# Kernel tuning notes

Hardware: AMD Instinct MI355X
Metric: run time of the kernel (lower is better)

Reference implementation:

```python
import jax, jax.numpy as jnp
import numpy as np

B, S, E, H, FF = 2, 2048, 768, 12, 3072
D = E // H
EPS = 1e-5


def setup_inputs() -> dict:
    key = jax.random.key(0)
    ks = jax.random.split(key, 12)
    sc = lambda n: 1.0 / np.sqrt(n)
    return {
        "x": jax.random.normal(ks[0], (B, S, E), jnp.float32),
        "wq": jax.random.normal(ks[1], (E, E), jnp.float32) * sc(E),
        "wk": jax.random.normal(ks[2], (E, E), jnp.float32) * sc(E),
        "wv": jax.random.normal(ks[3], (E, E), jnp.float32) * sc(E),
        "wo": jax.random.normal(ks[4], (E, E), jnp.float32) * sc(E),
        "bo": jax.random.normal(ks[5], (E,), jnp.float32) * 0.02,
        "w1": jax.random.normal(ks[6], (FF, E), jnp.float32) * sc(E),
        "b1": jax.random.normal(ks[7], (FF,), jnp.float32) * 0.02,
        "w2": jax.random.normal(ks[8], (E, FF), jnp.float32) * sc(FF),
        "b2": jax.random.normal(ks[9], (E,), jnp.float32) * 0.02,
        "gamma": jnp.ones((E,), jnp.float32),
        "beta": jnp.zeros((E,), jnp.float32),
    }


def _layernorm(x, g, b):
    mu = jnp.mean(x, axis=-1, keepdims=True)
    var = jnp.mean(jnp.square(x - mu), axis=-1, keepdims=True)
    return (x - mu) * jax.lax.rsqrt(var + EPS) * g + b


def reference(x, wq, wk, wv, wo, bo, w1, b1, w2, b2, gamma, beta):
    res = x
    xn = _layernorm(x, gamma, beta)
    # Q/K/V projections (torch Linear: y = x @ W.T), split into heads
    q = (xn @ wq.T).reshape(B, S, H, D)
    k = (xn @ wk.T).reshape(B, S, H, D)
    v = (xn @ wv.T).reshape(B, S, H, D)
    scale = jnp.sqrt(jnp.float32(D))
    scores = jnp.einsum("bqhd,bkhd->bhqk", q, k) / scale  # [B,H,S,S]
    causal = jnp.tril(jnp.ones((S, S), bool))
    scores = jnp.where(causal, scores, -jnp.inf)
    w = jax.nn.softmax(scores, axis=-1)
    attn = jnp.einsum("bhqk,bkhd->bqhd", w, v).reshape(B, S, E)
    attn = attn @ wo.T + bo
    res = res + attn
    y = _layernorm(res, gamma, beta)  # NOTE: same LayerNorm params reused (as in source)
    h = jax.nn.gelu(y @ w1.T + b1, approximate=False)  # nn.GELU default is exact erf
    ffn = h @ w2.T + b2
    return res + ffn
```

## Files before the change

### kernel.cpp

```cpp
#include <hip/hip_runtime.h>
#include <hip/hip_bf16.h>
#include <math.h>

typedef __bf16 bf16_8 __attribute__((ext_vector_type(8)));
typedef __bf16 bf16_4 __attribute__((ext_vector_type(4)));
typedef float f32x4 __attribute__((ext_vector_type(4)));

#define AS1 __attribute__((address_space(1)))
#define AS3 __attribute__((address_space(3)))

__global__ __launch_bounds__(256) void ln_kernel(
    const float* __restrict__ x, const float* __restrict__ g,
    const float* __restrict__ b, __hip_bfloat16* __restrict__ out, int cols) {
  const int row = blockIdx.x;
  const int t = threadIdx.x;
  float loc[3];
  float s = 0.f, s2 = 0.f;
#pragma unroll
  for (int i = 0; i < 3; ++i) {
    float v = x[(size_t)row * cols + t + i * 256];
    loc[i] = v;
    s += v;
    s2 += v * v;
  }
#pragma unroll
  for (int off = 32; off; off >>= 1) {
    s += __shfl_down(s, off);
    s2 += __shfl_down(s2, off);
  }
  __shared__ float red[2][4];
  const int lane = t & 63, w = t >> 6;
  if (lane == 0) {
    red[0][w] = s;
    red[1][w] = s2;
  }
  __syncthreads();
  s = red[0][0] + red[0][1] + red[0][2] + red[0][3];
  s2 = red[1][0] + red[1][1] + red[1][2] + red[1][3];
  const float mu = s / cols;
  const float var = s2 / cols - mu * mu;
  const float rs = rsqrtf(var + 1e-5f);
  __hip_bfloat16* orow = out + (size_t)row * cols;
#pragma unroll
  for (int i = 0; i < 3; ++i) {
    int c = t + i * 256;
    orow[c] = __hip_bfloat16((loc[i] - mu) * rs * g[c] + b[c]);
  }
}

__global__ __launch_bounds__(256) void reduce_ln(
    const float* __restrict__ x, const float* __restrict__ part, int nz,
    const float* __restrict__ bias, const float* __restrict__ g,
    const float* __restrict__ b, float* __restrict__ res,
    __hip_bfloat16* __restrict__ yout) {
  const int row = blockIdx.x;
  const int t = threadIdx.x;
  const size_t zstride = (size_t)4096 * 768;
  float loc[3];
  float s = 0.f, s2 = 0.f;
#pragma unroll
  for (int i = 0; i < 3; ++i) {
    const int c = t + i * 256;
    const size_t off = (size_t)row * 768 + c;
    float v = x[off] + bias[c];
    for (int z = 0; z < nz; ++z) v += part[(size_t)z * zstride + off];
    res[off] = v;
    loc[i] = v;
    s += v;
    s2 += v * v;
  }
#pragma unroll
  for (int off = 32; off; off >>= 1) {
    s += __shfl_down(s, off);
    s2 += __shfl_down(s2, off);
  }
  __shared__ float red[2][4];
  const int lane = t & 63, w = t >> 6;
  if (lane == 0) {
    red[0][w] = s;
    red[1][w] = s2;
  }
  __syncthreads();
  s = red[0][0] + red[0][1] + red[0][2] + red[0][3];
  s2 = red[1][0] + red[1][1] + red[1][2] + red[1][3];
  const float mu = s / 768.f;
  const float var = s2 / 768.f - mu * mu;
  const float rs = rsqrtf(var + 1e-5f);
#pragma unroll
  for (int i = 0; i < 3; ++i) {
    const int c = t + i * 256;
    yout[(size_t)row * 768 + c] = __hip_bfloat16((loc[i] - mu) * rs * g[c] + b[c]);
  }
}

__global__ __launch_bounds__(256) void reduce_out(
    const float* __restrict__ part, int nz, const float* __restrict__ bias,
    float* __restrict__ res) {
  const int row = blockIdx.x;
  const int t = threadIdx.x;
  const size_t zstride = (size_t)4096 * 768;
#pragma unroll
  for (int i = 0; i < 3; ++i) {
    const int c = t + i * 256;
    const size_t off = (size_t)row * 768 + c;
    float v = res[off] + bias[c];
    for (int z = 0; z < nz; ++z) v += part[(size_t)z * zstride + off];
    res[off] = v;
  }
}

__global__ __launch_bounds__(256) void cvt_multi(
    const float* __restrict__ sa, const float* __restrict__ sb,
    const float* __restrict__ sc, const float* __restrict__ sd,
    __hip_bfloat16* __restrict__ da, __hip_bfloat16* __restrict__ db,
    __hip_bfloat16* __restrict__ dc, __hip_bfloat16* __restrict__ dd) {
  const float* src;
  __hip_bfloat16* dst;
  if (blockIdx.y == 0) { src = sa; dst = da; }
  else if (blockIdx.y == 1) { src = sb; dst = db; }
  else if (blockIdx.y == 2) { src = sc; dst = dc; }
  else { src = sd; dst = dd; }
  const size_t i = ((size_t)blockIdx.x * 256 + threadIdx.x) * 4;
  float4 f = *(const float4*)(src + i);
  bf16_4 o;
  o[0] = (__bf16)f.x; o[1] = (__bf16)f.y; o[2] = (__bf16)f.z; o[3] = (__bf16)f.w;
  *(bf16_4*)((__bf16*)dst + i) = o;
}

__global__ __launch_bounds__(256) void transpose_v(
    const __hip_bfloat16* __restrict__ v, __hip_bfloat16* __restrict__ vt) {
  const int S = 2048, E = 768, H = 12;
  const int s0 = blockIdx.x * 64;
  const int bh = blockIdx.y;
  const int b = bh / H, h = bh - b * H;
  __shared__ __align__(16) __bf16 T[64 * 72];
  const int tid = threadIdx.x;
#pragma unroll
  for (int u = 0; u < 2; ++u) {
    int i = tid + u * 256;
    int sr = i >> 3, c = i & 7;
    *(bf16_8*)(&T[sr * 72 + c * 8]) =
        *(const bf16_8*)(v + ((size_t)b * S + s0 + sr) * E + h * 64 + c * 8);
  }
  __syncthreads();
#pragma unroll
  for (int u = 0; u < 2; ++u) {
    int i = tid + u * 256;
    int dr = i >> 3, kc = i & 7;
    bf16_8 o;
#pragma unroll
    for (int e = 0; e < 8; ++e) o[e] = T[(kc * 8 + e) * 72 + dr];
    *(bf16_8*)(vt + ((size_t)bh * 64 + dr) * S + s0 + kc * 8) = o;
  }
}

template <int MODE, bool BF32>
__global__ __launch_bounds__(256) void gemm_bt(
    const __hip_bfloat16* __restrict__ A, const void* __restrict__ Bx,
    const float* __restrict__ bias, void* __restrict__ out,
    int M, int N, int K, int lda, int ldb, int ldout) {
  constexpr int BM = 128, BN = 128, BK = 64;
  constexpr int LDBP = BF32 ? 72 : BK;
  __shared__ __align__(16) __bf16 As[2][BM * BK];
  __shared__ __align__(16) __bf16 Bs[2][BN * LDBP];
  const int tid = threadIdx.x;
  const int m0 = blockIdx.y * BM;
  const int n0 = blockIdx.x * BN;
  const int wave = tid >> 6;
  const int lane = tid & 63;
  const int quad = lane >> 4;
  const int l16 = lane & 15;
  const int wm = (wave & 1) * 64;
  const int wn = (wave >> 1) * 64;

  int kbase = 0, kcnt = K;
  if constexpr (MODE == 2 || MODE == 3) {
    kcnt = K / gridDim.z;
    kbase = blockIdx.z * kcnt;
  }
  const int nt = kcnt / BK;

  const int srow = lane >> 3;
  const int scol = ((lane & 7) ^ (srow & 7)) * 8;
  const __hip_bfloat16* Ap = A + (size_t)(m0 + wave * 8 + srow) * lda + kbase + scol;
  const __hip_bfloat16* Bpb = nullptr;
  const float* Bpf = nullptr;
  if constexpr (BF32)
    Bpf = (const float*)Bx;
  else
    Bpb = (const __hip_bfloat16*)Bx + (size_t)(n0 + wave * 8 + srow) * ldb + kbase + scol;

  f32x4 acc[4][4] = {};

  auto STAGE = [&](int t, int buf) {
    const int k0 = t * BK;
#pragma unroll
    for (int u = 0; u < 4; ++u) {
      __builtin_amdgcn_global_load_lds(
          (const AS1 void*)(Ap + (size_t)(u * 32) * lda + k0),
          (AS3 void*)(&As[buf][(u * 32 + wave * 8) * BK]), 16, 0, 0);
      if constexpr (!BF32)
        __builtin_amdgcn_global_load_lds(
            (const AS1 void*)(Bpb + (size_t)(u * 32) * ldb + k0),
            (AS3 void*)(&Bs[buf][(u * 32 + wave * 8) * BK]), 16, 0, 0);
    }
    if constexpr (BF32) {
#pragma unroll
      for (int u = 0; u < 4; ++u) {
        int c = u * 256 + tid;
        int row = c >> 3, kc = c & 7;
        const float* src = Bpf + (size_t)(n0 + row) * ldb + kbase + k0 + kc * 8;
        float4 f0 = *(const float4*)src;
        float4 f1 = *(const float4*)(src + 4);
        bf16_8 bv;
        bv[0] = (__bf16)f0.x; bv[1] = (__bf16)f0.y; bv[2] = (__bf16)f0.z; bv[3] = (__bf16)f0.w;
        bv[4] = (__bf16)f1.x; bv[5] = (__bf16)f1.y; bv[6] = (__bf16)f1.z; bv[7] = (__bf16)f1.w;
        *(bf16_8*)(&Bs[buf][row * LDBP + kc * 8]) = bv;
      }
    }
  };

  STAGE(0, 0);
  __syncthreads();
  int cur = 0;
  for (int t = 0; t < nt; ++t) {
    if (t + 1 < nt) STAGE(t + 1, cur ^ 1);
#pragma unroll
    for (int kk = 0; kk < 2; ++kk) {
      bf16_8 af[4], bfr[4];
#pragma unroll
      for (int i = 0; i < 4; ++i)
        af[i] = *(const bf16_8*)(
            &As[cur][(wm + i * 16 + l16) * BK + (((kk * 4 + quad) ^ (l16 & 7)) * 8)]);
#pragma unroll
      for (int j = 0; j < 4; ++j) {
        if constexpr (BF32)
          bfr[j] = *(const bf16_8*)(&Bs[cur][(wn + j * 16 + l16) * LDBP + kk * 32 + quad * 8]);
        else
          bfr[j] = *(const bf16_8*)(
              &Bs[cur][(wn + j * 16 + l16) * BK + (((kk * 4 + quad) ^ (l16 & 7)) * 8)]);
      }
#pragma unroll
      for (int i = 0; i < 4; ++i)
#pragma unroll
        for (int j = 0; j < 4; ++j)
          acc[i][j] =
              __builtin_amdgcn_mfma_f32_16x16x32_bf16(af[i], bfr[j], acc[i][j], 0, 0, 0);
    }
    __syncthreads();
    cur ^= 1;
  }

#pragma unroll
  for (int i = 0; i < 4; ++i) {
#pragma unroll
    for (int j = 0; j < 4; ++j) {
#pragma unroll
      for (int r = 0; r < 4; ++r) {
        const int row = m0 + wm + i * 16 + quad * 4 + r;
        const int col = n0 + wn + j * 16 + l16;
        const float v = acc[i][j][r];
        if constexpr (MODE == 0) {
          const int tsel = n0 / 768;
          const size_t idx = ((size_t)tsel * M + row) * 768 + (col - tsel * 768);
          ((__hip_bfloat16*)out)[idx] = __hip_bfloat16(v);
        } else if constexpr (MODE == 1) {
          float tt = v + bias[col];
          float gl = 0.5f * tt * (1.0f + erff(tt * 0.70710678118654752f));
          ((__hip_bfloat16*)out)[(size_t)row * ldout + col] = __hip_bfloat16(gl);
        } else if constexpr (MODE == 2) {
          float add = v + ((blockIdx.z == 0 && bias) ? bias[col] : 0.f);
          atomicAdd((float*)out + (size_t)row * 768 + col, add);
        } else {
          ((float*)out)[(size_t)blockIdx.z * M * 768 + (size_t)row * 768 + col] = v;
        }
      }
    }
  }
}

__global__ void zero_ctr(int* __restrict__ c) {
  if (threadIdx.x == 0) *c = 0;
}

#define ALDP 72
template <bool PRE_T>
__global__ __launch_bounds__(256) void attn_mfma(
    const __hip_bfloat16* __restrict__ qb, const __hip_bfloat16* __restrict__ kb,
    const __hip_bfloat16* __restrict__ vb, __hip_bfloat16* __restrict__ ob,
    int* __restrict__ ctr) {
  const int S = 2048, H = 12, E = 768;
  const int tid = threadIdx.x;
  const int wave = tid >> 6;
  const int lane = tid & 63;
  const int quad = lane >> 4;
  const int l16 = lane & 15;

  __shared__ __align__(16) __bf16 Ks[2][64 * 64];
  __shared__ __align__(16) __bf16 Vt[2][64 * 64];
  __shared__ __align__(16) __bf16 Pl[4][16 * ALDP];
  __shared__ int task;

  const int srow8 = lane >> 3;
  const int csrc = ((lane & 7) ^ srow8) * 8;

  for (;;) {
    if (tid == 0) task = atomicAdd(ctr, 1);
    __syncthreads();
    const int t = task;
    if (t >= 24 * 32) return;
    const int qblk = 31 - (t / 24);
    const int bh = t - (t / 24) * 24;
    const int b = bh / H, h = bh - b * H;
    const int q0 = qblk * 64;
    const int qw = q0 + wave * 16;
    const size_t base = (size_t)b * S * E + (size_t)h * 64;

    auto STAGE = [&](int kts, int buf) {
      const int k0s = kts * 64;
#pragma unroll
      for (int u = 0; u < 2; ++u) {
        const int trow = wave * 16 + u * 8;
        __builtin_amdgcn_global_load_lds(
            (const AS1 void*)(kb + base + (size_t)(k0s + trow + srow8) * E + csrc),
            (AS3 void*)(&Ks[buf][trow * 64]), 16, 0, 0);
        if constexpr (PRE_T)
          __builtin_amdgcn_global_load_lds(
              (const AS1 void*)(vb + ((size_t)(bh * 64 + trow + srow8)) * S + k0s + csrc),
              (AS3 void*)(&Vt[buf][trow * 64]), 16, 0, 0);
      }
      if constexpr (!PRE_T) {
#pragma unroll
        for (int u = 0; u < 2; ++u) {
          int i = tid + u * 256;
          int kr = i & 63, dq = i >> 6;
          bf16_8 vv = *(const bf16_8*)(vb + base + (size_t)(k0s + kr) * E + dq * 8);
#pragma unroll
          for (int j = 0; j < 8; ++j) {
            int drow = dq * 8 + j;
            Vt[buf][drow * 64 + (((kr >> 3) ^ (drow & 7)) * 8) + (kr & 7)] = vv[j];
          }
        }
      }
    };

    bf16_8 qf[2];
#pragma unroll
    for (int s = 0; s < 2; ++s)
      qf[s] = *(const bf16_8*)(qb + base + (size_t)(qw + l16) * E + s * 32 + quad * 8);

    f32x4 o[4] = {};
    float mq = -1e30f, lq = 0.f;

    STAGE(0, 0);
    __syncthreads();
    int cur = 0;

    for (int kt = 0; kt <= qblk; ++kt) {
      const int k0 = kt * 64;
      if (kt < qblk) STAGE(kt + 1, cur ^ 1);

      f32x4 sc[4] = {};
      __builtin_amdgcn_s_setprio(1);
#pragma unroll
      for (int jj = 0; jj < 4; ++jj)
#pragma unroll
        for (int s = 0; s < 2; ++s) {
          bf16_8 kf = *(const bf16_8*)(
              &Ks[cur][(jj * 16 + l16) * 64 + (((s * 4 + quad) ^ (l16 & 7)) * 8)]);
          sc[jj] = __builtin_amdgcn_mfma_f32_16x16x32_bf16(kf, qf[s], sc[jj], 0, 0, 0);
        }
      __builtin_amdgcn_s_setprio(0);

      float mx = -1e30f;
#pragma unroll
      for (int jj = 0; jj < 4; ++jj)
#pragma unroll
        for (int r = 0; r < 4; ++r) {
          float v = sc[jj][r] * 0.125f;
          if (kt == qblk && (k0 + jj * 16 + quad * 4 + r) > (qw + l16)) v = -1e30f;
          sc[jj][r] = v;
          mx = fmaxf(mx, v);
        }
      mx = fmaxf(mx, __shfl_xor(mx, 16));
      mx = fmaxf(mx, __shfl_xor(mx, 32));
      const float mn = fmaxf(mq, mx);
      const float corr = __expf(mq - mn);
      mq = mn;
      float sum = 0.f;
#pragma unroll
      for (int jj = 0; jj < 4; ++jj)
#pragma unroll
        for (int r = 0; r < 4; ++r) {
          float p = __expf(sc[jj][r] - mn);
          sc[jj][r] = p;
          sum += p;
        }
      sum += __shfl_xor(sum, 16);
      sum += __shfl_xor(sum, 32);
      lq = lq * corr + sum;
#pragma unroll
      for (int nt2 = 0; nt2 < 4; ++nt2)
#pragma unroll
        for (int r = 0; r < 4; ++r) o[nt2][r] *= corr;

      __bf16* pw = &Pl[wave][0];
#pragma unroll
      for (int jj = 0; jj < 4; ++jj) {
        bf16_4 p4;
#pragma unroll
        for (int r = 0; r < 4; ++r) p4[r] = (__bf16)sc[jj][r];
        *(bf16_4*)(&pw[l16 * ALDP + jj * 16 + quad * 4]) = p4;
      }

#pragma unroll
      for (int s = 0; s < 2; ++s) {
        bf16_8 pf = *(const bf16_8*)(&pw[l16 * ALDP + s * 32 + quad * 8]);
        __builtin_amdgcn_s_setprio(1);
#pragma unroll
        for (int dt = 0; dt < 4; ++dt) {
          bf16_8 vf = *(const bf16_8*)(
              &Vt[cur][(dt * 16 + l16) * 64 + (((s * 4 + quad) ^ (l16 & 7)) * 8)]);
          o[dt] = __builtin_amdgcn_mfma_f32_16x16x32_bf16(vf, pf, o[dt], 0, 0, 0);
        }
        __builtin_amdgcn_s_setprio(0);
      }

      __syncthreads();
      cur ^= 1;
    }

    const float inv = 1.f / lq;
    __bf16* pw = &Pl[wave][0];
#pragma unroll
    for (int dt = 0; dt < 4; ++dt) {
      bf16_4 o4;
#pragma unroll
      for (int r = 0; r < 4; ++r) o4[r] = (__bf16)(o[dt][r] * inv);
      *(bf16_4*)(&pw[l16 * ALDP + dt * 16 + quad * 4]) = o4;
    }
#pragma unroll
    for (int u = 0; u < 2; ++u) {
      int j = lane + u * 64;
      int ql = j >> 3, ch = j & 7;
      bf16_8 ov = *(const bf16_8*)(&pw[ql * ALDP + ch * 8]);
      *(bf16_8*)(ob + base + (size_t)(qw + ql) * E + ch * 8) = ov;
    }
  }
}

extern "C" void kernel_launch(void* const* d_in, const int* in_sizes, int n_in,
                              void* d_out, int out_size, void* d_ws, size_t ws_size,
                              hipStream_t stream) {
  const int Bv = 2, S = 2048, E = 768, FF = 3072;
  const int M = Bv * S;
  const size_t ME = (size_t)M * E;
  const size_t EE = (size_t)E * E;
  const size_t EF = (size_t)E * FF;

  const float* x = (const float*)d_in[0];
  const float* wq = (const float*)d_in[1];
  const float* wk = (const float*)d_in[2];
  const float* wv = (const float*)d_in[3];
  const float* wo = (const float*)d_in[4];
  const float* bo = (const float*)d_in[5];
  const float* w1 = (const float*)d_in[6];
  const float* b1 = (const float*)d_in[7];
  const float* w2 = (const float*)d_in[8];
  const float* b2 = (const float*)d_in[9];
  const float* gamma = (const float*)d_in[10];
  const float* beta = (const float*)d_in[11];

  int* ctr = (int*)d_ws;
  __hip_bfloat16* slot = (__hip_bfloat16*)((char*)d_ws + 256);
  __hip_bfloat16* s0 = slot;
  __hip_bfloat16* s1 = slot + ME;
  __hip_bfloat16* s4 = slot + 4 * ME;
  __hip_bfloat16* s5 = slot + 5 * ME;
  float* pp = (float*)(slot + 5 * ME + 2 * EF);
  __hip_bfloat16* vt = (__hip_bfloat16*)pp;
  float* res = (float*)d_out;

  const size_t need_mid = 256 + (5 * ME + 2 * EF) * sizeof(__hip_bfloat16);
  const size_t need_full = need_mid + 4 * ME * sizeof(float);
  const bool full = ws_size >= need_full;
  const bool mid = ws_size >= need_mid;

  cvt_multi<<<dim3(EE / 1024, 4), 256, 0, stream>>>(
      wq, wk, wv, wo, s4, s4 + EE, s4 + 2 * EE, s4 + 3 * EE);
  if (mid)
    cvt_multi<<<dim3(EF / 1024, 2), 256, 0, stream>>>(
        w1, w2, nullptr, nullptr, s5, s5 + EF, nullptr, nullptr);
  ln_kernel<<<M, 256, 0, stream>>>(x, gamma, beta, s0, E);
  gemm_bt<0, false><<<dim3(18, 32), 256, 0, stream>>>(s0, s4, nullptr, s1, M, 2304, E, E, E, 0);
  zero_ctr<<<1, 64, 0, stream>>>(ctr);
  if (full) {
    transpose_v<<<dim3(32, 24), 256, 0, stream>>>(s1 + 2 * ME, vt);
    attn_mfma<true><<<768, 256, 0, stream>>>(s1, s1 + ME, vt, s0, ctr);
  } else {
    attn_mfma<false><<<768, 256, 0, stream>>>(s1, s1 + ME, s1 + 2 * ME, s0, ctr);
  }

  if (full) {
    gemm_bt<3, false><<<dim3(6, 32, 4), 256, 0, stream>>>(
        s0, s4 + 3 * EE, nullptr, pp, M, E, E, E, E, 0);
    reduce_ln<<<M, 256, 0, stream>>>(x, pp, 4, bo, gamma, beta, res, s0);
    gemm_bt<1, false><<<dim3(24, 32), 256, 0, stream>>>(s0, s5, b1, s1, M, FF, E, E, E, FF);
    gemm_bt<3, false><<<dim3(6, 32, 4), 256, 0, stream>>>(
        s1, s5 + EF, nullptr, pp, M, E, FF, FF, FF, 0);
    reduce_out<<<M, 256, 0, stream>>>(pp, 4, b2, res);
  } else {
    hipMemcpyAsync(d_out, x, ME * sizeof(float), hipMemcpyDeviceToDevice, stream);
    gemm_bt<2, false><<<dim3(6, 32, 2), 256, 0, stream>>>(
        s0, s4 + 3 * EE, bo, res, M, E, E, E, E, 0);
    ln_kernel<<<M, 256, 0, stream>>>(res, gamma, beta, s0, E);
    if (mid) {
      gemm_bt<1, false><<<dim3(24, 32), 256, 0, stream>>>(s0, s5, b1, s1, M, FF, E, E, E, FF);
      gemm_bt<2, false><<<dim3(6, 32, 4), 256, 0, stream>>>(
          s1, s5 + EF, b2, res, M, E, FF, FF, FF, 0);
    } else {
      gemm_bt<1, true><<<dim3(24, 32), 256, 0, stream>>>(s0, w1, b1, s1, M, FF, E, E, E, FF);
      cvt_multi<<<dim3(EF / 1024, 1), 256, 0, stream>>>(
          w2, nullptr, nullptr, nullptr, s0, nullptr, nullptr, nullptr);
      gemm_bt<2, false><<<dim3(6, 32, 4), 256, 0, stream>>>(
          s1, s0, b2, res, M, E, FF, FF, FF, 0);
    }
  }
}
```

Measured before the change: 332.8 us.

## Keep attention probabilities in registers by permuting V key order

Permutes the key ordering of the transposed V tile, both in the pre-transpose kernel and in the in-kernel staging path, so the score MFMA output layout matches the B-operand layout of the PV MFMA. Probabilities can then be packed to bf16 directly in registers instead of round-tripping through a per-wave LDS buffer. That buffer is removed, and the epilogue reuses the Ks buffer for output staging. Softmax switches to exp2 with the scale folded into log2e, and the causal mask is applied only on the diagonal tile. The main risks are mismatched permutations producing wrong results and a hazard from reusing Ks after the final barrier.

```diff
diff --git a/kernel.cpp b/kernel.cpp
--- a/kernel.cpp
+++ b/kernel.cpp
@@ -149,7 +149,10 @@
     int dr = i >> 3, kc = i & 7;
     bf16_8 o;
 #pragma unroll
-    for (int e = 0; e < 8; ++e) o[e] = T[(kc * 8 + e) * 72 + dr];
+    for (int e = 0; e < 8; ++e) {
+      int k = 32 * (kc >> 2) + 16 * (e >> 2) + 4 * (kc & 3) + (e & 3);
+      o[e] = T[k * 72 + dr];
+    }
     *(bf16_8*)(vt + ((size_t)bh * 64 + dr) * S + s0 + kc * 8) = o;
   }
 }
@@ -298,11 +301,13 @@
 
   __shared__ __align__(16) __bf16 Ks[2][64 * 64];
   __shared__ __align__(16) __bf16 Vt[2][64 * 64];
-  __shared__ __align__(16) __bf16 Pl[4][16 * ALDP];
   __shared__ int task;
+  __bf16* ep = &Ks[0][0] + wave * 16 * ALDP;
 
   const int srow8 = lane >> 3;
   const int csrc = ((lane & 7) ^ srow8) * 8;
+
+  const float SCL = 0.18033688011112042f;
 
   for (;;) {
     if (tid == 0) task = atomicAdd(ctr, 1);
@@ -335,10 +340,11 @@
           int i = tid + u * 256;
           int kr = i & 63, dq = i >> 6;
           bf16_8 vv = *(const bf16_8*)(vb + base + (size_t)(k0s + kr) * E + dq * 8);
+          const int c = 32 * (kr >> 5) + 8 * ((kr >> 2) & 3) + 4 * ((kr >> 4) & 1) + (kr & 3);
 #pragma unroll
           for (int j = 0; j < 8; ++j) {
             int drow = dq * 8 + j;
-            Vt[buf][drow * 64 + (((kr >> 3) ^ (drow & 7)) * 8) + (kr & 7)] = vv[j];
+            Vt[buf][drow * 64 + (((c >> 3) ^ (drow & 7)) * 8) + (c & 7)] = vv[j];
           }
         }
       }
@@ -372,30 +378,35 @@
         }
       __builtin_amdgcn_s_setprio(0);
 
-      float mx = -1e30f;
 #pragma unroll
       for (int jj = 0; jj < 4; ++jj)
 #pragma unroll
-        for (int r = 0; r < 4; ++r) {
-          float v = sc[jj][r] * 0.125f;
-          if (kt == qblk && (k0 + jj * 16 + quad * 4 + r) > (qw + l16)) v = -1e30f;
-          sc[jj][r] = v;
-          mx = fmaxf(mx, v);
-        }
+        for (int r = 0; r < 4; ++r) sc[jj][r] *= SCL;
+      if (kt == qblk) {
+#pragma unroll
+        for (int jj = 0; jj < 4; ++jj)
+#pragma unroll
+          for (int r = 0; r < 4; ++r)
+            if ((k0 + jj * 16 + quad * 4 + r) > (qw + l16)) sc[jj][r] = -1e30f;
+      }
+      float mj[4];
+#pragma unroll
+      for (int jj = 0; jj < 4; ++jj)
+        mj[jj] = fmaxf(fmaxf(sc[jj][0], sc[jj][1]), fmaxf(sc[jj][2], sc[jj][3]));
+      float mx = fmaxf(fmaxf(mj[0], mj[1]), fmaxf(mj[2], mj[3]));
       mx = fmaxf(mx, __shfl_xor(mx, 16));
       mx = fmaxf(mx, __shfl_xor(mx, 32));
       const float mn = fmaxf(mq, mx);
-      const float corr = __expf(mq - mn);
+      const float corr = exp2f(mq - mn);
       mq = mn;
-      float sum = 0.f;
-#pragma unroll
-      for (int jj = 0; jj < 4; ++jj)
-#pragma unroll
-        for (int r = 0; r < 4; ++r) {
-          float p = __expf(sc[jj][r] - mn);
-          sc[jj][r] = p;
-          sum += p;
-        }
+      float sj[4];
+#pragma unroll
+      for (int jj = 0; jj < 4; ++jj) {
+#pragma unroll
+        for (int r = 0; r < 4; ++r) sc[jj][r] = exp2f(sc[jj][r] - mn);
+        sj[jj] = (sc[jj][0] + sc[jj][1]) + (sc[jj][2] + sc[jj][3]);
+      }
+      float sum = (sj[0] + sj[1]) + (sj[2] + sj[3]);
       sum += __shfl_xor(sum, 16);
       sum += __shfl_xor(sum, 32);
       lq = lq * corr + sum;
@@ -404,46 +415,43 @@
 #pragma unroll
         for (int r = 0; r < 4; ++r) o[nt2][r] *= corr;
 
-      __bf16* pw = &Pl[wave][0];
-#pragma unroll
-      for (int jj = 0; jj < 4; ++jj) {
-        bf16_4 p4;
-#pragma unroll
-        for (int r = 0; r < 4; ++r) p4[r] = (__bf16)sc[jj][r];
-        *(bf16_4*)(&pw[l16 * ALDP + jj * 16 + quad * 4]) = p4;
-      }
-
-#pragma unroll
-      for (int s = 0; s < 2; ++s) {
-        bf16_8 pf = *(const bf16_8*)(&pw[l16 * ALDP + s * 32 + quad * 8]);
-        __builtin_amdgcn_s_setprio(1);
+      bf16_8 pf[2];
+#pragma unroll
+      for (int s = 0; s < 2; ++s)
+#pragma unroll
+        for (int r = 0; r < 4; ++r) {
+          pf[s][r] = (__bf16)sc[2 * s][r];
+          pf[s][4 + r] = (__bf16)sc[2 * s + 1][r];
+        }
+
+      __builtin_amdgcn_s_setprio(1);
+#pragma unroll
+      for (int s = 0; s < 2; ++s)
 #pragma unroll
         for (int dt = 0; dt < 4; ++dt) {
           bf16_8 vf = *(const bf16_8*)(
               &Vt[cur][(dt * 16 + l16) * 64 + (((s * 4 + quad) ^ (l16 & 7)) * 8)]);
-          o[dt] = __builtin_amdgcn_mfma_f32_16x16x32_bf16(vf, pf, o[dt], 0, 0, 0);
+          o[dt] = __builtin_amdgcn_mfma_f32_16x16x32_bf16(vf, pf[s], o[dt], 0, 0, 0);
         }
-        __builtin_amdgcn_s_setprio(0);
-      }
+      __builtin_amdgcn_s_setprio(0);
 
       __syncthreads();
       cur ^= 1;
     }
 
     const float inv = 1.f / lq;
-    __bf16* pw = &Pl[wave][0];
 #pragma unroll
     for (int dt = 0; dt < 4; ++dt) {
       bf16_4 o4;
 #pragma unroll
       for (int r = 0; r < 4; ++r) o4[r] = (__bf16)(o[dt][r] * inv);
-      *(bf16_4*)(&pw[l16 * ALDP + dt * 16 + quad * 4]) = o4;
+      *(bf16_4*)(&ep[l16 * ALDP + dt * 16 + quad * 4]) = o4;
     }
 #pragma unroll
     for (int u = 0; u < 2; ++u) {
       int j = lane + u * 64;
       int ql = j >> 3, ch = j & 7;
-      bf16_8 ov = *(const bf16_8*)(&pw[ql * ALDP + ch * 8]);
+      bf16_8 ov = *(const bf16_8*)(&ep[ql * ALDP + ch * 8]);
       *(bf16_8*)(ob + base + (size_t)(qw + ql) * E + ch * 8) = ov;
     }
   }
```

Measured after the change: 330.8 us. Within noise of the previous version (-0.6%).
